# Kernel tuning notes

Measured on AMD Instinct MI355X. Metric: run time of the kernel, lower is better.

The kernel has to match this reference:

```python
import jax, jax.numpy as jnp
import numpy as np
from jax import lax

B, T, D, FF, E, TOPK, CLS = 16, 512, 1024, 2048, 4, 2, 1200
KW = 3  # conv kernel width per ff_kernelsize=[3,3]


def _sinusoidal_pe(T, D):
    pos = np.arange(T, dtype=np.float32)[:, None]
    div = np.exp(np.arange(0, D, 2, dtype=np.float32) * (-np.log(10000.0) / D))
    pe = np.zeros((T, D), dtype=np.float32)
    pe[:, 0::2] = np.sin(pos * div)
    pe[:, 1::2] = np.cos(pos * div)
    return jnp.asarray(pe)


def setup_inputs() -> dict:
    key = jax.random.key(0)
    ks = jax.random.split(key, 12)
    sc = 0.02
    x = jax.random.normal(ks[0], (B, T, D), jnp.float32)
    mask = jax.random.randint(ks[1], (B, T), 0, 2).astype(jnp.int32)
    mask = mask.at[:, 0].set(1)  # ensure >=1 valid token
    return {
        "x": x,
        "mask": mask,
        "fc1_w": jax.random.normal(ks[2], (D, D), jnp.float32) * sc,
        "fc1_b": jnp.zeros((D,), jnp.float32),
        "bn_g": jnp.ones((D,), jnp.float32),
        "bn_b": jnp.zeros((D,), jnp.float32),
        "pe": _sinusoidal_pe(T, D),
        "gate_w": jax.random.normal(ks[3], (D, E), jnp.float32) * sc,
        "ew1": jax.random.normal(ks[4], (E, FF, D, KW), jnp.float32) * sc,  # OIH per expert
        "eb1": jnp.zeros((E, FF), jnp.float32),
        "ew2": jax.random.normal(ks[5], (E, D, FF, KW), jnp.float32) * sc,
        "eb2": jnp.zeros((E, D), jnp.float32),
        "ln_g": jnp.ones((D,), jnp.float32),
        "ln_b": jnp.zeros((D,), jnp.float32),
        "out_w": jax.random.normal(ks[6], (CLS, D), jnp.float32) * sc,
        "out_b": jnp.zeros((CLS,), jnp.float32),
    }


def _forward(x, mask, fc1_w, fc1_b, bn_g, bn_b, pe, gate_w, ew1, eb1, ew2, eb2, ln_g, ln_b, out_w, out_b):
    mf = mask.astype(x.dtype)[..., None]  # [B,T,1]

    # fc1
    h = jnp.einsum("btd,ed->bte", x, fc1_w) + fc1_b

    # MaskedNorm (batch): stats over valid tokens only, invalid positions passed through
    cnt = jnp.maximum(jnp.sum(mf), 1.0)
    mean = jnp.sum(h * mf, axis=(0, 1)) / cnt
    var = jnp.sum(mf * (h - mean) ** 2, axis=(0, 1)) / cnt
    normed = (h - mean) * lax.rsqrt(var + 1e-5) * bn_g + bn_b
    h = jnp.where(mf > 0, normed, h)

    # ReLU + positional encoding (+ dropout is identity in eval)
    h = jax.nn.relu(h) + pe[None, :, :]

    # --- MoE with top-2 gating over 4 conv-FFN experts ---
    logits_g = jnp.einsum("btd,de->bte", h, gate_w)  # [B,T,E]
    probs_g = jax.nn.softmax(logits_g, axis=-1)
    top_v, top_i = lax.top_k(logits_g, TOPK)  # [B,T,K]
    top_g = jax.nn.softmax(top_v, axis=-1)
    # scatter top-k gates into dense [B,T,E] (E=4, cheap)
    gates = jnp.sum(top_g[..., None] * jax.nn.one_hot(top_i, E, dtype=h.dtype), axis=2)

    ht = jnp.transpose(h, (0, 2, 1))  # [B,D,T] for NCH conv

    def expert(w1, b1, w2, b2):
        y = lax.conv_general_dilated(ht, w1, (1,), "SAME", dimension_numbers=("NCH", "OIH", "NCH"))
        y = jax.nn.relu(y + b1[None, :, None])
        y = lax.conv_general_dilated(y, w2, (1,), "SAME", dimension_numbers=("NCH", "OIH", "NCH"))
        return y + b2[None, :, None]  # [B,D,T]

    ys = jax.vmap(expert)(ew1, eb1, ew2, eb2)  # [E,B,D,T]
    moe_out = jnp.einsum("bte,ebdt->btd", gates, ys)

    # load-balancing aux loss (Switch-style)
    frac = jnp.mean((gates > 0).astype(h.dtype), axis=(0, 1))  # tokens per expert
    imp = jnp.mean(probs_g, axis=(0, 1))
    aux_loss = E * jnp.sum(frac * imp)

    # LayerNorm (eps 1e-6)
    mu = jnp.mean(moe_out, axis=-1, keepdims=True)
    v = jnp.mean((moe_out - mu) ** 2, axis=-1, keepdims=True)
    feat = (moe_out - mu) * lax.rsqrt(v + 1e-6) * ln_g + ln_b

    logits = jnp.einsum("btd,cd->btc", feat, out_w) + out_b
    logp = jax.nn.log_softmax(logits, axis=2)
    p = jnp.exp(logp)
    feat_norm = feat / jnp.maximum(jnp.linalg.norm(feat, axis=-1, keepdims=True), 1e-12)
    return feat, feat_norm, logits, logp, p, aux_loss


def reference(x, mask, fc1_w, fc1_b, bn_g, bn_b, pe, gate_w, ew1, eb1, ew2, eb2, ln_g, ln_b, out_w, out_b):
    return _forward(x, mask, fc1_w, fc1_b, bn_g, bn_b, pe, gate_w, ew1, eb1, ew2, eb2, ln_g, ln_b, out_w, out_b)
```

## Files before the change

kernel.cpp:

```cpp
#include <hip/hip_runtime.h>
#include <hip/hip_bf16.h>


namespace {

constexpr int kB = 16, kT = 512, kD = 1024, kFF = 2048, kE = 4, kCLS = 1200;
constexpr int kM = kB * kT;
constexpr int kTP = kT + 2;
constexpr int kCLSP = 1280;
constexpr size_t kBTD = (size_t)kM * kD;
constexpr size_t kBTC = (size_t)kM * kCLS;
constexpr size_t kY1S = (size_t)kB * kTP * kFF;
constexpr size_t kTapStride = (size_t)kFF * kD;

constexpr size_t WS_H     = 0;
constexpr size_t WS_HPAD  = WS_H + kBTD;
constexpr size_t WS_Y1P   = WS_HPAD + (size_t)kB * kTP * kD / 2;
constexpr size_t WS_W1T   = WS_Y1P + (size_t)kB * kTP * kFF / 2;
constexpr size_t WS_W2T   = WS_W1T + (size_t)3 * kFF * kD / 2;
constexpr size_t WS_GATES = WS_W2T + (size_t)3 * kD * kFF / 2;
constexpr size_t WS_PROBS = WS_GATES + (size_t)kM * kE;
constexpr size_t WS_W1HI  = WS_PROBS + (size_t)kM * kE;
constexpr size_t WS_W1LO  = WS_W1HI + (size_t)kD * kD / 2;
constexpr size_t WS_OWB   = WS_W1LO + (size_t)kD * kD / 2;
constexpr size_t WS_SUMS  = WS_OWB + (size_t)kCLSP * kD / 2;
constexpr size_t WS_SUMSQ = WS_SUMS + kD;
constexpr size_t WS_CNT   = WS_SUMSQ + kD;
constexpr size_t WS_AA    = WS_CNT + 1;
constexpr size_t WS_CC    = WS_AA + kD;
constexpr int WS_ZERON = (int)(2 * kD + 1);

constexpr size_t BW_H     = 0;
constexpr size_t BW_HPAD  = BW_H + kBTD;
constexpr size_t BW_Y1    = BW_HPAD + (size_t)kB * kTP * kD / 2;
constexpr size_t BW_W1T   = BW_Y1 + (size_t)kE * kY1S / 2;
constexpr size_t BW_W2T   = BW_W1T + (size_t)kE * 3 * kFF * kD / 2;
constexpr size_t BW_GATES = BW_W2T + (size_t)kE * 3 * kD * kFF / 2;
constexpr size_t BW_PROBS = BW_GATES + (size_t)kM * kE;
constexpr size_t BW_W1HI  = BW_PROBS + (size_t)kM * kE;
constexpr size_t BW_W1LO  = BW_W1HI + (size_t)kD * kD / 2;
constexpr size_t BW_OWB   = BW_W1LO + (size_t)kD * kD / 2;
constexpr size_t BW_SUMS  = BW_OWB + (size_t)kCLSP * kD / 2;
constexpr size_t BW_SUMSQ = BW_SUMS + kD;
constexpr size_t BW_CNT   = BW_SUMSQ + kD;
constexpr size_t BW_AA    = BW_CNT + 1;
constexpr size_t BW_CC    = BW_AA + kD;
constexpr size_t BW_ECNT  = BW_CC + kD;
constexpr size_t BW_ELIST = BW_ECNT + 4;
constexpr size_t BW_END   = BW_ELIST + (size_t)kE * kM;

typedef __attribute__((ext_vector_type(8))) short short8;
typedef __attribute__((ext_vector_type(4))) float f32x4;

#define GLOBAL_LOAD_LDS16(gp, lp)                                          \
  __builtin_amdgcn_global_load_lds(                                        \
      (const __attribute__((address_space(1))) void*)(gp),                 \
      (__attribute__((address_space(3))) void*)(lp), 16, 0, 0)

__device__ __forceinline__ float block_reduce_sum(float v, float* red) {
  const int tid = threadIdx.x;
  __syncthreads();
  red[tid] = v;
  __syncthreads();
  for (int s = 128; s > 0; s >>= 1) {
    if (tid < s) red[tid] += red[tid + s];
    __syncthreads();
  }
  return red[0];
}

__device__ __forceinline__ float block_reduce_max(float v, float* red) {
  const int tid = threadIdx.x;
  __syncthreads();
  red[tid] = v;
  __syncthreads();
  for (int s = 128; s > 0; s >>= 1) {
    if (tid < s) red[tid] = fmaxf(red[tid], red[tid + s]);
    __syncthreads();
  }
  return red[0];
}

__global__ void k_zero(float* __restrict__ p, int n) {
  int i = blockIdx.x * 256 + threadIdx.x;
  if (i < n) p[i] = 0.f;
}

__global__ void k_zero_bnd(__hip_bfloat16* __restrict__ Hpad,
                           __hip_bfloat16* __restrict__ Y1pad) {
  const int b = blockIdx.x >> 1;
  const int row = b * kTP + ((blockIdx.x & 1) ? (kTP - 1) : 0);
  const __hip_bfloat16 z = __float2bfloat16(0.f);
  for (int d = threadIdx.x; d < kD; d += 256) Hpad[(size_t)row * kD + d] = z;
  for (int d = threadIdx.x; d < kFF; d += 256) Y1pad[(size_t)row * kFF + d] = z;
}

__global__ void k_zero_bnd_all(__hip_bfloat16* __restrict__ Hpad,
                               __hip_bfloat16* __restrict__ Y1all) {
  const int g = blockIdx.x;
  const int which = g / (2 * kB);
  const int r = g % (2 * kB);
  const int b = r >> 1;
  const int row = b * kTP + ((r & 1) ? (kTP - 1) : 0);
  const __hip_bfloat16 z = __float2bfloat16(0.f);
  if (which == 0) {
    for (int d = threadIdx.x; d < kD; d += 256) Hpad[(size_t)row * kD + d] = z;
  } else {
    __hip_bfloat16* Y = Y1all + (size_t)(which - 1) * kY1S;
    for (int d = threadIdx.x; d < kFF; d += 256) Y[(size_t)row * kFF + d] = z;
  }
}

__global__ __launch_bounds__(256) void k_split(const float* __restrict__ src,
                                               __hip_bfloat16* __restrict__ hi,
                                               __hip_bfloat16* __restrict__ lo,
                                               int n4) {
  const int i = blockIdx.x * 256 + threadIdx.x;
  if (i >= n4) return;
  const float4 v = *reinterpret_cast<const float4*>(src + (size_t)i * 4);
  const float vv[4] = {v.x, v.y, v.z, v.w};
  unsigned short h[4], l[4];
#pragma unroll
  for (int j = 0; j < 4; ++j) {
    __hip_bfloat16 hb = __float2bfloat16(vv[j]);
    __hip_bfloat16 lb = __float2bfloat16(vv[j] - __bfloat162float(hb));
    h[j] = *reinterpret_cast<unsigned short*>(&hb);
    l[j] = *reinterpret_cast<unsigned short*>(&lb);
  }
  *reinterpret_cast<short4*>(hi + (size_t)i * 4) =
      make_short4(h[0], h[1], h[2], h[3]);
  *reinterpret_cast<short4*>(lo + (size_t)i * 4) =
      make_short4(l[0], l[1], l[2], l[3]);
}

__global__ __launch_bounds__(256) void k_wcast_pad(
    const float* __restrict__ w, __hip_bfloat16* __restrict__ dst) {
  const size_t i = (size_t)blockIdx.x * 256 + threadIdx.x;
  if (i >= (size_t)kCLSP * kD) return;
  const size_t r = i / kD;
  dst[i] = __float2bfloat16(r < kCLS ? w[i] : 0.f);
}

__global__ __launch_bounds__(256) void k_wt(const float* __restrict__ src,
                                            __hip_bfloat16* __restrict__ dst,
                                            int n) {
  const int i = blockIdx.x * 256 + threadIdx.x;
  if (i >= n) return;
  const float* s = src + (size_t)i * 3;
  dst[i] = __float2bfloat16(s[0]);
  dst[(size_t)n + i] = __float2bfloat16(s[1]);
  dst[(size_t)2 * n + i] = __float2bfloat16(s[2]);
}

__global__ __launch_bounds__(256) void k_wt_all(const float* __restrict__ ew1,
                                                const float* __restrict__ ew2,
                                                __hip_bfloat16* __restrict__ W1T,
                                                __hip_bfloat16* __restrict__ W2T) {
  const size_t n = (size_t)kFF * kD;
  const size_t total = (size_t)kE * n;
  const size_t i = (size_t)blockIdx.x * 256 + threadIdx.x;
  if (i >= total) return;
  const size_t e = i / n, j = i - e * n;
  {
    const float* s = ew1 + (e * n + j) * 3;
    __hip_bfloat16* d = W1T + e * 3 * n;
    d[j] = __float2bfloat16(s[0]);
    d[n + j] = __float2bfloat16(s[1]);
    d[2 * n + j] = __float2bfloat16(s[2]);
  }
  {
    const float* s = ew2 + (e * n + j) * 3;
    __hip_bfloat16* d = W2T + e * 3 * n;
    d[j] = __float2bfloat16(s[0]);
    d[n + j] = __float2bfloat16(s[1]);
    d[2 * n + j] = __float2bfloat16(s[2]);
  }
}

__global__ __launch_bounds__(256) void k_build_elist(
    const float* __restrict__ gates, int* __restrict__ elist,
    int* __restrict__ ecnt) {
  __shared__ int red[256];
  const int e = blockIdx.x;
  const int tid = threadIdx.x;
  const int base = tid * 32;
  int cnt = 0;
  for (int j = 0; j < 32; ++j)
    if (gates[(size_t)(base + j) * 4 + e] > 0.f) ++cnt;
  red[tid] = cnt;
  __syncthreads();
  for (int s = 1; s < 256; s <<= 1) {
    const int v = (tid >= s) ? red[tid - s] : 0;
    __syncthreads();
    red[tid] += v;
    __syncthreads();
  }
  const int total = red[255];
  int pos = red[tid] - cnt;
  int* dst = elist + (size_t)e * kM;
  for (int j = 0; j < 32; ++j) {
    const int tk = base + j;
    if (gates[(size_t)tk * 4 + e] > 0.f) dst[pos++] = tk;
  }
  const int padded = (total + 255) & ~255;
  for (int i = total + tid; i < padded; i += 256) dst[i] = 0;
  if (tid == 0) ecnt[e] = total;
}

__global__ __launch_bounds__(256) void k_fc1_mfma(
    const __hip_bfloat16* __restrict__ Xhi, const __hip_bfloat16* __restrict__ Xlo,
    const __hip_bfloat16* __restrict__ Whi, const __hip_bfloat16* __restrict__ Wlo,
    const float* __restrict__ bias, float* __restrict__ H) {
  __shared__ __align__(16) __hip_bfloat16 As[128 * 32];
  __shared__ __align__(16) __hip_bfloat16 Bs[128 * 32];
  const int tid = threadIdx.x;
  const int m0 = blockIdx.y * 128;
  const int n0 = blockIdx.x * 128;
  const int w = tid >> 6, lane = tid & 63;
  const int wm = (w >> 1) * 64, wn = (w & 1) * 64;
  f32x4 acc[4][4] = {};
  const int fr = lane & 15, fc = (lane >> 4) * 8;
  const __hip_bfloat16* Aps[3] = {Xhi, Xlo, Xhi};
  const __hip_bfloat16* Bps[3] = {Whi, Whi, Wlo};
  for (int p = 0; p < 3; ++p) {
    const __hip_bfloat16* Ab = Aps[p] + (size_t)m0 * kD;
    const __hip_bfloat16* Bb = Bps[p] + (size_t)n0 * kD;
    for (int k0 = 0; k0 < kD; k0 += 32) {
      __syncthreads();
#pragma unroll
      for (int r = 0; r < 2; ++r) {
        const int idx = r * 256 + tid;
        const int row = idx >> 2, cg = (idx & 3) * 8;
        GLOBAL_LOAD_LDS16(Ab + (size_t)row * kD + k0 + cg, &As[idx * 8]);
        GLOBAL_LOAD_LDS16(Bb + (size_t)row * kD + k0 + cg, &Bs[idx * 8]);
      }
      __syncthreads();
      short8 af[4], bf[4];
#pragma unroll
      for (int i = 0; i < 4; ++i) {
        af[i] = *reinterpret_cast<const short8*>(&As[(wm + i * 16 + fr) * 32 + fc]);
        bf[i] = *reinterpret_cast<const short8*>(&Bs[(wn + i * 16 + fr) * 32 + fc]);
      }
#pragma unroll
      for (int i = 0; i < 4; ++i)
#pragma unroll
        for (int j = 0; j < 4; ++j)
          acc[i][j] = __builtin_amdgcn_mfma_f32_16x16x32_bf16(af[i], bf[j], acc[i][j], 0, 0, 0);
    }
  }
  const int cr = (lane >> 4) * 4, cc = lane & 15;
#pragma unroll
  for (int i = 0; i < 4; ++i) {
#pragma unroll
    for (int r = 0; r < 4; ++r) {
      const int m = m0 + wm + i * 16 + cr + r;
#pragma unroll
      for (int j = 0; j < 4; ++j) {
        const int gc = n0 + wn + j * 16 + cc;
        H[(size_t)m * kD + gc] = acc[i][j][r] + bias[gc];
      }
    }
  }
}

__global__ __launch_bounds__(256) void k_cls_mfma(
    const __hip_bfloat16* __restrict__ Fb, const __hip_bfloat16* __restrict__ Wb,
    const float* __restrict__ bias, float* __restrict__ logits) {
  __shared__ __align__(16) __hip_bfloat16 As[128 * 32];
  __shared__ __align__(16) __hip_bfloat16 Bs[128 * 32];
  const int tid = threadIdx.x;
  const int m0 = blockIdx.y * 128;
  const int n0 = blockIdx.x * 128;
  const int w = tid >> 6, lane = tid & 63;
  const int wm = (w >> 1) * 64, wn = (w & 1) * 64;
  f32x4 acc[4][4] = {};
  const int fr = lane & 15, fc = (lane >> 4) * 8;
  const __hip_bfloat16* Ab = Fb + (size_t)m0 * kD;
  const __hip_bfloat16* Bb = Wb + (size_t)n0 * kD;
  for (int k0 = 0; k0 < kD; k0 += 32) {
    __syncthreads();
#pragma unroll
    for (int r = 0; r < 2; ++r) {
      const int idx = r * 256 + tid;
      const int row = idx >> 2, cg = (idx & 3) * 8;
      GLOBAL_LOAD_LDS16(Ab + (size_t)row * kD + k0 + cg, &As[idx * 8]);
      GLOBAL_LOAD_LDS16(Bb + (size_t)row * kD + k0 + cg, &Bs[idx * 8]);
    }
    __syncthreads();
    short8 af[4], bf[4];
#pragma unroll
    for (int i = 0; i < 4; ++i) {
      af[i] = *reinterpret_cast<const short8*>(&As[(wm + i * 16 + fr) * 32 + fc]);
      bf[i] = *reinterpret_cast<const short8*>(&Bs[(wn + i * 16 + fr) * 32 + fc]);
    }
#pragma unroll
    for (int i = 0; i < 4; ++i)
#pragma unroll
      for (int j = 0; j < 4; ++j)
        acc[i][j] = __builtin_amdgcn_mfma_f32_16x16x32_bf16(af[i], bf[j], acc[i][j], 0, 0, 0);
  }
  const int cr = (lane >> 4) * 4, cc = lane & 15;
#pragma unroll
  for (int i = 0; i < 4; ++i) {
#pragma unroll
    for (int r = 0; r < 4; ++r) {
      const int m = m0 + wm + i * 16 + cr + r;
#pragma unroll
      for (int j = 0; j < 4; ++j) {
        const int gc = n0 + wn + j * 16 + cc;
        if (gc < kCLS) logits[(size_t)m * kCLS + gc] = acc[i][j][r] + bias[gc];
      }
    }
  }
}

__global__ __launch_bounds__(256) void k_conv1_mfma(
    const __hip_bfloat16* __restrict__ Hpad, const __hip_bfloat16* __restrict__ W1T,
    const float* __restrict__ b1, __hip_bfloat16* __restrict__ Y1pad) {
  __shared__ __align__(16) __hip_bfloat16 As[128 * 32];
  __shared__ __align__(16) __hip_bfloat16 Bs[128 * 32];
  const int tid = threadIdx.x;
  const int m0 = blockIdx.y * 128;
  const int n0 = blockIdx.x * 128;
  const int b = m0 >> 9;
  const int t0 = m0 & (kT - 1);
  const int arow0 = b * kTP + t0;
  const int w = tid >> 6, lane = tid & 63;
  const int wm = (w >> 1) * 64, wn = (w & 1) * 64;
  f32x4 acc[4][4] = {};
  const int fr = lane & 15, fc = (lane >> 4) * 8;
  for (int kk = 0; kk < 3; ++kk) {
    const __hip_bfloat16* Ab = Hpad + (size_t)(arow0 + kk) * kD;
    const __hip_bfloat16* Bb = W1T + (size_t)kk * kFF * kD + (size_t)n0 * kD;
    for (int k0 = 0; k0 < kD; k0 += 32) {
      __syncthreads();
#pragma unroll
      for (int r = 0; r < 2; ++r) {
        const int idx = r * 256 + tid;
        const int row = idx >> 2, cg = (idx & 3) * 8;
        GLOBAL_LOAD_LDS16(Ab + (size_t)row * kD + k0 + cg, &As[idx * 8]);
        GLOBAL_LOAD_LDS16(Bb + (size_t)row * kD + k0 + cg, &Bs[idx * 8]);
      }
      __syncthreads();
      short8 af[4], bf[4];
#pragma unroll
      for (int i = 0; i < 4; ++i) {
        af[i] = *reinterpret_cast<const short8*>(&As[(wm + i * 16 + fr) * 32 + fc]);
        bf[i] = *reinterpret_cast<const short8*>(&Bs[(wn + i * 16 + fr) * 32 + fc]);
      }
#pragma unroll
      for (int i = 0; i < 4; ++i)
#pragma unroll
        for (int j = 0; j < 4; ++j)
          acc[i][j] = __builtin_amdgcn_mfma_f32_16x16x32_bf16(af[i], bf[j], acc[i][j], 0, 0, 0);
    }
  }
  const int orow0 = b * kTP + t0 + 1;
  const int cr = (lane >> 4) * 4, cc = lane & 15;
#pragma unroll
  for (int i = 0; i < 4; ++i) {
#pragma unroll
    for (int r = 0; r < 4; ++r) {
      const int lr = wm + i * 16 + cr + r;
#pragma unroll
      for (int j = 0; j < 4; ++j) {
        const int gc = n0 + wn + j * 16 + cc;
        const float v = acc[i][j][r] + b1[gc];
        Y1pad[(size_t)(orow0 + lr) * kFF + gc] = __float2bfloat16(fmaxf(v, 0.f));
      }
    }
  }
}

__global__ __launch_bounds__(256) void k_conv2_mfma(
    const __hip_bfloat16* __restrict__ Y1pad, const __hip_bfloat16* __restrict__ W2T,
    const float* __restrict__ b2, const float* __restrict__ gates,
    int e, float* __restrict__ moe) {
  __shared__ __align__(16) __hip_bfloat16 As[128 * 32];
  __shared__ __align__(16) __hip_bfloat16 Bs[128 * 32];
  const int tid = threadIdx.x;
  const int m0 = blockIdx.y * 128;
  const int n0 = blockIdx.x * 128;
  const int b = m0 >> 9;
  const int t0 = m0 & (kT - 1);
  const int arow0 = b * kTP + t0;
  const int w = tid >> 6, lane = tid & 63;
  const int wm = (w >> 1) * 64, wn = (w & 1) * 64;
  f32x4 acc[4][4] = {};
  const int fr = lane & 15, fc = (lane >> 4) * 8;
  for (int kk = 0; kk < 3; ++kk) {
    const __hip_bfloat16* Ab = Y1pad + (size_t)(arow0 + kk) * kFF;
    const __hip_bfloat16* Bb = W2T + (size_t)kk * kD * kFF + (size_t)n0 * kFF;
    for (int k0 = 0; k0 < kFF; k0 += 32) {
      __syncthreads();
#pragma unroll
      for (int r = 0; r < 2; ++r) {
        const int idx = r * 256 + tid;
        const int row = idx >> 2, cg = (idx & 3) * 8;
        GLOBAL_LOAD_LDS16(Ab + (size_t)row * kFF + k0 + cg, &As[idx * 8]);
        GLOBAL_LOAD_LDS16(Bb + (size_t)row * kFF + k0 + cg, &Bs[idx * 8]);
      }
      __syncthreads();
      short8 af[4], bf[4];
#pragma unroll
      for (int i = 0; i < 4; ++i) {
        af[i] = *reinterpret_cast<const short8*>(&As[(wm + i * 16 + fr) * 32 + fc]);
        bf[i] = *reinterpret_cast<const short8*>(&Bs[(wn + i * 16 + fr) * 32 + fc]);
      }
#pragma unroll
      for (int i = 0; i < 4; ++i)
#pragma unroll
        for (int j = 0; j < 4; ++j)
          acc[i][j] = __builtin_amdgcn_mfma_f32_16x16x32_bf16(af[i], bf[j], acc[i][j], 0, 0, 0);
    }
  }
  const int cr = (lane >> 4) * 4, cc = lane & 15;
#pragma unroll
  for (int i = 0; i < 4; ++i) {
#pragma unroll
    for (int r = 0; r < 4; ++r) {
      const int lr = wm + i * 16 + cr + r;
      const int m = m0 + lr;
      const float g = gates[(size_t)m * kE + e];
#pragma unroll
      for (int j = 0; j < 4; ++j) {
        const int gc = n0 + wn + j * 16 + cc;
        const float v = acc[i][j][r] + b2[gc];
        const size_t idx = (size_t)m * kD + gc;
        moe[idx] = (e == 0 ? 0.f : moe[idx]) + g * v;
      }
    }
  }
}

#define WAITBAR(N)                                  \
  do {                                              \
    asm volatile("s_waitcnt vmcnt(" #N ")");        \
    __builtin_amdgcn_s_barrier();                   \
    __builtin_amdgcn_sched_barrier(0);              \
  } while (0)

#define QUAD(D, MH, NH, LOADA)                                                \
  do {                                                                        \
    const int _d = (D);                                                       \
    if (LOADA) {                                                              \
      const int _ab = ((_d * 2 + (MH)) << 14) + (fr << 6) + (fc << 1);        \
      _Pragma("unroll") for (int _i = 0; _i < 4; ++_i)                        \
          _Pragma("unroll") for (int _ks = 0; _ks < 2; ++_ks)                 \
              areg[_i][_ks] = *reinterpret_cast<const short8*>(               \
                  smem + ((_ab + (((wr * 4 + _i) * 2 + _ks) << 10)) ^ aswz)); \
    }                                                                         \
    short8 breg[2][2];                                                        \
    const int _bb =                                                           \
        65536 + ((_d * 2 + (NH)) << 14) + (fr << 6) + (fc << 1);              \
    _Pragma("unroll") for (int _j = 0; _j < 2; ++_j)                          \
        _Pragma("unroll") for (int _ks = 0; _ks < 2; ++_ks)                   \
            breg[_j][_ks] = *reinterpret_cast<const short8*>(                 \
                smem + ((_bb + (((wc * 2 + _j) * 2 + _ks) << 10)) ^ aswz));   \
    __builtin_amdgcn_s_setprio(1);                                            \
    _Pragma("unroll") for (int _i = 0; _i < 4; ++_i)                          \
        _Pragma("unroll") for (int _j = 0; _j < 2; ++_j)                      \
            _Pragma("unroll") for (int _ks = 0; _ks < 2; ++_ks)               \
                acc[MH][NH][_i][_j] =                                         \
                    __builtin_amdgcn_mfma_f32_16x16x32_bf16(                  \
                        areg[_i][_ks], breg[_j][_ks], acc[MH][NH][_i][_j],    \
                        0, 0, 0);                                             \
    __builtin_amdgcn_s_setprio(0);                                            \
  } while (0)

template <int K1, bool CONV1>
__global__ __launch_bounds__(512, 2) void k_conv8ph(
    const __hip_bfloat16* __restrict__ Asrc,
    const __hip_bfloat16* __restrict__ Wt,
    const float* __restrict__ bias,
    const float* __restrict__ gates,
    __hip_bfloat16* __restrict__ Yout,
    float* __restrict__ moe) {
  constexpr int NTOT = CONV1 ? kFF : kD;
  constexpr int NX = NTOT / 256;
  constexpr int NY = kM / 256;
  constexpr int NWG = kE * NY * NX;
  constexpr int KT1 = K1 / 64;
  constexpr int NT = 3 * KT1;
  extern __shared__ __align__(16) char smem[];

  int lid = blockIdx.x;
  lid = (lid & 7) * (NWG / 8) + (lid >> 3);
  const int e = lid / (NY * NX);
  const int rem = lid - e * (NY * NX);
  const int by = rem / NX, bx = rem - by * NX;
  const int m0 = by * 256, n0 = bx * 256;
  const int b = m0 >> 9, t0 = m0 & (kT - 1);
  const int arow0 = b * kTP + t0;

  const int tid = threadIdx.x;
  const int w = tid >> 6, l = tid & 63;
  const int wr = w >> 2, wc = w & 3;
  const int fr = l & 15, fc = (l >> 4) << 3;
  const int aswz = (fr & 8) ? 32 : 0;
  const int srr = l >> 2;
  const int scc = ((l & 3) << 3) ^ ((l & 32) ? 16 : 0);

  const __hip_bfloat16* Apan =
      (CONV1 ? Asrc : (Asrc + (size_t)e * kY1S)) + (size_t)arow0 * K1;
  const __hip_bfloat16* Bpan = Wt + (size_t)e * 3 * kTapStride + (size_t)n0 * K1;

  auto stageA = [&](int tau, int d, int mh) {
    const int kk = tau / KT1, kf = (tau % KT1) << 6;
    const __hip_bfloat16* org = Apan + (size_t)(kk + mh * 128) * K1 + kf;
    const int lb = (d * 2 + mh) << 14;
#pragma unroll
    for (int r = 0; r < 2; ++r) {
      const int s = w + r * 8;
      GLOBAL_LOAD_LDS16(org + (size_t)((s >> 1) * 16 + srr) * K1 +
                            ((s & 1) << 5) + scc,
                        smem + lb + (s << 10));
    }
  };
  auto stageB = [&](int tau, int d, int nh) {
    const int kk = tau / KT1, kf = (tau % KT1) << 6;
    const __hip_bfloat16* org =
        Bpan + (size_t)kk * kTapStride + (size_t)(nh * 128) * K1 + kf;
    const int lb = 65536 + ((d * 2 + nh) << 14);
#pragma unroll
    for (int r = 0; r < 2; ++r) {
      const int s = w + r * 8;
      GLOBAL_LOAD_LDS16(org + (size_t)((s >> 1) * 16 + srr) * K1 +
                            ((s & 1) << 5) + scc,
                        smem + lb + (s << 10));
    }
  };

  f32x4 acc[2][2][4][2] = {};
  short8 areg[4][2];

  stageA(0, 0, 0);
  stageB(0, 0, 0);
  stageB(0, 0, 1);
  stageA(0, 0, 1);

  for (int tau = 0; tau < NT - 1; ++tau) {
    const int d = tau & 1, dn = d ^ 1;
    WAITBAR(4); stageA(tau + 1, dn, 0); QUAD(d, 0, 0, true);
    WAITBAR(4); stageB(tau + 1, dn, 0); QUAD(d, 0, 1, false);
    WAITBAR(4); stageB(tau + 1, dn, 1); QUAD(d, 1, 0, true);
                stageA(tau + 1, dn, 1); QUAD(d, 1, 1, false);
  }
  {
    const int d = (NT - 1) & 1;
    WAITBAR(4); QUAD(d, 0, 0, true);
    WAITBAR(2); QUAD(d, 0, 1, false);
    WAITBAR(0); QUAD(d, 1, 0, true);
                QUAD(d, 1, 1, false);
  }

  const int cr = (l >> 4) * 4, cc = l & 15;
  if (CONV1) {
    __hip_bfloat16* Yb = Yout + (size_t)e * kY1S;
    const float* be = bias + (size_t)e * kFF;
    const int orow0 = b * kTP + t0 + 1;
#pragma unroll
    for (int mh = 0; mh < 2; ++mh)
#pragma unroll
      for (int i = 0; i < 4; ++i)
#pragma unroll
        for (int r = 0; r < 4; ++r) {
          const int rl = mh * 128 + wr * 64 + i * 16 + cr + r;
#pragma unroll
          for (int nh = 0; nh < 2; ++nh)
#pragma unroll
            for (int j = 0; j < 2; ++j) {
              const int gc = n0 + nh * 128 + wc * 32 + j * 16 + cc;
              const float v = acc[mh][nh][i][j][r] + be[gc];
              Yb[(size_t)(orow0 + rl) * kFF + gc] =
                  __float2bfloat16(fmaxf(v, 0.f));
            }
        }
  } else {
    const float* be = bias + (size_t)e * kD;
#pragma unroll
    for (int mh = 0; mh < 2; ++mh)
#pragma unroll
      for (int i = 0; i < 4; ++i)
#pragma unroll
        for (int r = 0; r < 4; ++r) {
          const int rl = mh * 128 + wr * 64 + i * 16 + cr + r;
          const int m = m0 + rl;
          const float g = gates[(size_t)m * kE + e];
#pragma unroll
          for (int nh = 0; nh < 2; ++nh)
#pragma unroll
            for (int j = 0; j < 2; ++j) {
              const int gc = n0 + nh * 128 + wc * 32 + j * 16 + cc;
              const float v = acc[mh][nh][i][j][r] + be[gc];
              atomicAdd(&moe[(size_t)m * kD + gc], g * v);
            }
        }
  }
}

__global__ __launch_bounds__(512, 2) void k_conv2sp(
    const __hip_bfloat16* __restrict__ Y1all,
    const __hip_bfloat16* __restrict__ W2T,
    const float* __restrict__ b2, const float* __restrict__ gates,
    const int* __restrict__ elist, const int* __restrict__ ecnt,
    float* __restrict__ moe) {
  constexpr int K1 = kFF;
  constexpr int NX = kD / 256;
  constexpr int NY = kM / 256;
  constexpr int NWG = kE * NY * NX;
  constexpr int KT1 = K1 / 64;
  constexpr int NT = 3 * KT1;
  extern __shared__ __align__(16) char smem[];

  int lid = blockIdx.x;
  lid = (lid & 7) * (NWG / 8) + (lid >> 3);
  const int e = lid / (NY * NX);
  const int rem = lid - e * (NY * NX);
  const int by = rem / NX, bx = rem - by * NX;
  const int m0 = by * 256, n0 = bx * 256;
  const int cnt_e = ecnt[e];
  if (m0 >= cnt_e) return;

  const int tid = threadIdx.x;
  const int w = tid >> 6, l = tid & 63;
  const int wr = w >> 2, wc = w & 3;
  const int fr = l & 15, fc = (l >> 4) << 3;
  const int aswz = (fr & 8) ? 32 : 0;
  const int srr = l >> 2;
  const int scc = ((l & 3) << 3) ^ ((l & 32) ? 16 : 0);

  const int* el = elist + (size_t)e * kM + m0;
  const __hip_bfloat16* Ye = Y1all + (size_t)e * kY1S;
  const __hip_bfloat16* Bpan =
      W2T + (size_t)e * 3 * kTapStride + (size_t)n0 * K1;

  const int colbits = ((w & 1) << 5) + scc;
  const int r0 = (w >> 1) * 16 + srr;
  const int r1 = r0 + 64;
  const __hip_bfloat16* aptr[2][2];
#pragma unroll
  for (int mh = 0; mh < 2; ++mh) {
    const int tk0 = el[mh * 128 + r0];
    const int tk1 = el[mh * 128 + r1];
    aptr[mh][0] = Ye +
        (size_t)((tk0 >> 9) * kTP + (tk0 & (kT - 1))) * K1 + colbits;
    aptr[mh][1] = Ye +
        (size_t)((tk1 >> 9) * kTP + (tk1 & (kT - 1))) * K1 + colbits;
  }

  auto stageA = [&](int tau, int d, int mh) {
    const int lb = (d * 2 + mh) << 14;
    GLOBAL_LOAD_LDS16(aptr[mh][0] + tau * 64, smem + lb + (w << 10));
    GLOBAL_LOAD_LDS16(aptr[mh][1] + tau * 64, smem + lb + ((w + 8) << 10));
  };
  auto stageB = [&](int tau, int d, int nh) {
    const int kk = tau / KT1, kf = (tau % KT1) << 6;
    const __hip_bfloat16* org =
        Bpan + (size_t)kk * kTapStride + (size_t)(nh * 128) * K1 + kf;
    const int lb = 65536 + ((d * 2 + nh) << 14);
#pragma unroll
    for (int r = 0; r < 2; ++r) {
      const int s = w + r * 8;
      GLOBAL_LOAD_LDS16(org + (size_t)((s >> 1) * 16 + srr) * K1 +
                            ((s & 1) << 5) + scc,
                        smem + lb + (s << 10));
    }
  };

  f32x4 acc[2][2][4][2] = {};
  short8 areg[4][2];

  stageA(0, 0, 0);
  stageB(0, 0, 0);
  stageB(0, 0, 1);
  stageA(0, 0, 1);

  for (int tau = 0; tau < NT - 1; ++tau) {
    const int d = tau & 1, dn = d ^ 1;
    WAITBAR(4); stageA(tau + 1, dn, 0); QUAD(d, 0, 0, true);
    WAITBAR(4); stageB(tau + 1, dn, 0); QUAD(d, 0, 1, false);
    WAITBAR(4); stageB(tau + 1, dn, 1); QUAD(d, 1, 0, true);
                stageA(tau + 1, dn, 1); QUAD(d, 1, 1, false);
  }
  {
    const int d = (NT - 1) & 1;
    WAITBAR(4); QUAD(d, 0, 0, true);
    WAITBAR(2); QUAD(d, 0, 1, false);
    WAITBAR(0); QUAD(d, 1, 0, true);
                QUAD(d, 1, 1, false);
  }

  const int cr = (l >> 4) * 4, cc = l & 15;
  const float* be = b2 + (size_t)e * kD;
#pragma unroll
  for (int mh = 0; mh < 2; ++mh)
#pragma unroll
    for (int i = 0; i < 4; ++i)
#pragma unroll
      for (int r = 0; r < 4; ++r) {
        const int rl = mh * 128 + wr * 64 + i * 16 + cr + r;
        if (m0 + rl < cnt_e) {
          const int tk = el[rl];
          const float g = gates[(size_t)tk * 4 + e];
#pragma unroll
          for (int nh = 0; nh < 2; ++nh)
#pragma unroll
            for (int j = 0; j < 2; ++j) {
              const int gc = n0 + nh * 128 + wc * 32 + j * 16 + cc;
              const float v = acc[mh][nh][i][j][r] + be[gc];
              atomicAdd(&moe[(size_t)tk * kD + gc], g * v);
            }
        }
      }
}

__global__ __launch_bounds__(256) void k_cnt(const int* __restrict__ mask,
                                             float* __restrict__ cnt) {
  __shared__ float red[256];
  const int i = blockIdx.x * 256 + threadIdx.x;
  float v = (float)mask[i];
  v = block_reduce_sum(v, red);
  if (threadIdx.x == 0) atomicAdd(cnt, v);
}

__global__ __launch_bounds__(256) void k_stats(const float* __restrict__ H,
                                               const int* __restrict__ mask,
                                               float* __restrict__ sums,
                                               float* __restrict__ sumsq) {
  const int ch = blockIdx.x * 256 + threadIdx.x;
  const int r0 = blockIdx.y * 64;
  float s = 0.f, q = 0.f;
  for (int r = r0; r < r0 + 64; ++r) {
    if (mask[r]) {
      const float v = H[(size_t)r * kD + ch];
      s += v;
      q += v * v;
    }
  }
  atomicAdd(&sums[ch], s);
  atomicAdd(&sumsq[ch], q);
}

__global__ __launch_bounds__(256) void k_finalize(
    const float* __restrict__ sums, const float* __restrict__ sumsq,
    const float* __restrict__ cntp, const float* __restrict__ bn_g,
    const float* __restrict__ bn_b, float* __restrict__ aa,
    float* __restrict__ cc) {
  const int d = blockIdx.x * 256 + threadIdx.x;
  const float cnt = fmaxf(*cntp, 1.f);
  const float mean = sums[d] / cnt;
  const float var = sumsq[d] / cnt - mean * mean;
  const float istd = rsqrtf(var + 1e-5f);
  const float a = bn_g[d] * istd;
  aa[d] = a;
  cc[d] = bn_b[d] - mean * a;
}

__global__ __launch_bounds__(256) void k_norm_gate(
    const float* __restrict__ H, const int* __restrict__ mask,
    const float* __restrict__ pe, const float* __restrict__ aa,
    const float* __restrict__ cc, const float* __restrict__ gw,
    __hip_bfloat16* __restrict__ Hpad, float* __restrict__ gates,
    float* __restrict__ probs) {
  __shared__ float red[256];
  __shared__ float glog[4];
  const int r = blockIdx.x;
  const int tid = threadIdx.x;
  const int b = r >> 9;
  const int t = r & (kT - 1);
  const bool mv = mask[r] != 0;
  const size_t orow = (size_t)(b * kTP + t + 1) * kD;
  float gl[4] = {0.f, 0.f, 0.f, 0.f};
#pragma unroll
  for (int j = 0; j < 4; ++j) {
    const int d = tid + j * 256;
    float v = H[(size_t)r * kD + d];
    if (mv) v = v * aa[d] + cc[d];
    v = fmaxf(v, 0.f) + pe[(size_t)t * kD + d];
    Hpad[orow + d] = __float2bfloat16(v);
    const float4 g = *reinterpret_cast<const float4*>(gw + (size_t)d * 4);
    gl[0] += v * g.x; gl[1] += v * g.y; gl[2] += v * g.z; gl[3] += v * g.w;
  }
  for (int e = 0; e < 4; ++e) {
    const float s = block_reduce_sum(gl[e], red);
    if (tid == 0) glog[e] = s;
  }
  __syncthreads();
  if (tid == 0) {
    float lg[4] = {glog[0], glog[1], glog[2], glog[3]};
    const float mx = fmaxf(fmaxf(lg[0], lg[1]), fmaxf(lg[2], lg[3]));
    float ex[4], s = 0.f;
#pragma unroll
    for (int e = 0; e < 4; ++e) { ex[e] = expf(lg[e] - mx); s += ex[e]; }
    int i0 = 0;
    for (int e = 1; e < 4; ++e) if (lg[e] > lg[i0]) i0 = e;
    int i1 = -1;
    for (int e = 0; e < 4; ++e) {
      if (e == i0) continue;
      if (i1 < 0 || lg[e] > lg[i1]) i1 = e;
    }
    const float g0 = 1.f / (1.f + expf(lg[i1] - lg[i0]));
    float gv[4] = {0.f, 0.f, 0.f, 0.f};
    gv[i0] = g0;
    gv[i1] = 1.f - g0;
    *reinterpret_cast<float4*>(gates + (size_t)r * 4) =
        make_float4(gv[0], gv[1], gv[2], gv[3]);
    const float inv_s = 1.f / s;
    *reinterpret_cast<float4*>(probs + (size_t)r * 4) =
        make_float4(ex[0] * inv_s, ex[1] * inv_s, ex[2] * inv_s, ex[3] * inv_s);
  }
}

__global__ __launch_bounds__(256) void k_ln(
    const float* __restrict__ moe, const float* __restrict__ g,
    const float* __restrict__ b, float* __restrict__ feat,
    float* __restrict__ featn, __hip_bfloat16* __restrict__ featb) {
  __shared__ float red[256];
  const int r = blockIdx.x;
  const int tid = threadIdx.x;
  float v[4];
  float s = 0.f, q = 0.f;
#pragma unroll
  for (int j = 0; j < 4; ++j) {
    v[j] = moe[(size_t)r * kD + tid + j * 256];
    s += v[j];
    q += v[j] * v[j];
  }
  const float sum = block_reduce_sum(s, red);
  const float mu = sum * (1.f / kD);
  const float sq = block_reduce_sum(q, red);
  const float var = sq * (1.f / kD) - mu * mu;
  const float istd = rsqrtf(var + 1e-6f);
  float f[4];
  float fs = 0.f;
#pragma unroll
  for (int j = 0; j < 4; ++j) {
    const int d = tid + j * 256;
    f[j] = (v[j] - mu) * istd * g[d] + b[d];
    feat[(size_t)r * kD + d] = f[j];
    featb[(size_t)r * kD + d] = __float2bfloat16(f[j]);
    fs += f[j] * f[j];
  }
  const float nrm2 = block_reduce_sum(fs, red);
  const float scale = 1.f / fmaxf(sqrtf(nrm2), 1e-12f);
#pragma unroll
  for (int j = 0; j < 4; ++j) {
    const int d = tid + j * 256;
    featn[(size_t)r * kD + d] = f[j] * scale;
  }
}

__global__ __launch_bounds__(256) void k_softmax(
    const float* __restrict__ logits, float* __restrict__ logp,
    float* __restrict__ p) {
  __shared__ float red[256];
  const int r = blockIdx.x;
  const int tid = threadIdx.x;
  float lv[5];
  float mx = -1e30f;
#pragma unroll
  for (int j = 0; j < 5; ++j) {
    const int c = tid + j * 256;
    if (c < kCLS) {
      lv[j] = logits[(size_t)r * kCLS + c];
      mx = fmaxf(mx, lv[j]);
    }
  }
  mx = block_reduce_max(mx, red);
  float s = 0.f;
#pragma unroll
  for (int j = 0; j < 5; ++j) {
    const int c = tid + j * 256;
    if (c < kCLS) s += expf(lv[j] - mx);
  }
  s = block_reduce_sum(s, red);
  const float lse = mx + logf(s);
#pragma unroll
  for (int j = 0; j < 5; ++j) {
    const int c = tid + j * 256;
    if (c < kCLS) {
      const float lp = lv[j] - lse;
      logp[(size_t)r * kCLS + c] = lp;
      p[(size_t)r * kCLS + c] = expf(lp);
    }
  }
}

__global__ __launch_bounds__(256) void k_aux(const float* __restrict__ probs,
                                             const float* __restrict__ gates,
                                             float* __restrict__ out) {
  __shared__ float red[256];
  const int tid = threadIdx.x;
  float si[4] = {0.f, 0.f, 0.f, 0.f};
  float sf[4] = {0.f, 0.f, 0.f, 0.f};
  for (int i = tid; i < kM; i += 256) {
    const float4 p = *reinterpret_cast<const float4*>(probs + (size_t)i * 4);
    const float4 g = *reinterpret_cast<const float4*>(gates + (size_t)i * 4);
    si[0] += p.x; si[1] += p.y; si[2] += p.z; si[3] += p.w;
    sf[0] += (g.x > 0.f) ? 1.f : 0.f;
    sf[1] += (g.y > 0.f) ? 1.f : 0.f;
    sf[2] += (g.z > 0.f) ? 1.f : 0.f;
    sf[3] += (g.w > 0.f) ? 1.f : 0.f;
  }
  float tot = 0.f;
  for (int e = 0; e < 4; ++e) {
    const float S = block_reduce_sum(si[e], red);
    const float F = block_reduce_sum(sf[e], red);
    tot += (F / (float)kM) * (S / (float)kM);
  }
  if (tid == 0) out[0] = (float)kE * tot;
}

}

extern "C" void kernel_launch(void* const* d_in, const int* in_sizes, int n_in,
                              void* d_out, int out_size, void* d_ws,
                              size_t ws_size, hipStream_t stream) {
  const float* x     = (const float*)d_in[0];
  const int*   mask  = (const int*)d_in[1];
  const float* fc1_w = (const float*)d_in[2];
  const float* fc1_b = (const float*)d_in[3];
  const float* bn_g  = (const float*)d_in[4];
  const float* bn_b  = (const float*)d_in[5];
  const float* pe    = (const float*)d_in[6];
  const float* gw    = (const float*)d_in[7];
  const float* ew1   = (const float*)d_in[8];
  const float* eb1   = (const float*)d_in[9];
  const float* ew2   = (const float*)d_in[10];
  const float* eb2   = (const float*)d_in[11];
  const float* ln_g  = (const float*)d_in[12];
  const float* ln_b  = (const float*)d_in[13];
  const float* out_w = (const float*)d_in[14];
  const float* out_b = (const float*)d_in[15];

  float* ws = (float*)d_ws;

  float* outf   = (float*)d_out;
  float* feat   = outf;
  float* featn  = outf + kBTD;
  float* logits = outf + 2 * kBTD;
  float* logp   = logits + kBTC;
  float* pprob  = logp + kBTC;
  float* aux    = pprob + kBTC;

  const bool batched = ws_size >= BW_END * sizeof(float);

  if (batched) {
    float* H     = ws + BW_H;
    __hip_bfloat16* HPAD  = (__hip_bfloat16*)(ws + BW_HPAD);
    __hip_bfloat16* Y1ALL = (__hip_bfloat16*)(ws + BW_Y1);
    __hip_bfloat16* XHI   = Y1ALL;
    __hip_bfloat16* XLO   = XHI + kBTD;
    __hip_bfloat16* FEATB = Y1ALL;
    __hip_bfloat16* W1T   = (__hip_bfloat16*)(ws + BW_W1T);
    __hip_bfloat16* W2T   = (__hip_bfloat16*)(ws + BW_W2T);
    float* GATES = ws + BW_GATES;
    float* PROBS = ws + BW_PROBS;
    __hip_bfloat16* W1HI = (__hip_bfloat16*)(ws + BW_W1HI);
    __hip_bfloat16* W1LO = (__hip_bfloat16*)(ws + BW_W1LO);
    __hip_bfloat16* OWB  = (__hip_bfloat16*)(ws + BW_OWB);
    float* SUMS  = ws + BW_SUMS;
    int*   ECNT  = (int*)(ws + BW_ECNT);
    int*   ELIST = (int*)(ws + BW_ELIST);
    float* MOE   = H;

    k_zero<<<dim3((WS_ZERON + 255) / 256), 256, 0, stream>>>(SUMS, WS_ZERON);
    k_split<<<dim3((int)(kBTD / 4 + 255) / 256), 256, 0, stream>>>(
        x, XHI, XLO, (int)(kBTD / 4));
    k_split<<<dim3((kD * kD / 4 + 255) / 256), 256, 0, stream>>>(
        fc1_w, W1HI, W1LO, kD * kD / 4);
    k_fc1_mfma<<<dim3(kD / 128, kM / 128), 256, 0, stream>>>(
        XHI, XLO, W1HI, W1LO, fc1_b, H);
    k_zero_bnd_all<<<dim3(2 * kB * (1 + kE)), 256, 0, stream>>>(HPAD, Y1ALL);
    k_wt_all<<<dim3((int)(((size_t)kE * kFF * kD + 255) / 256)), 256, 0,
               stream>>>(ew1, ew2, W1T, W2T);
    k_cnt<<<dim3(kM / 256), 256, 0, stream>>>(mask, ws + BW_CNT);
    k_stats<<<dim3(kD / 256, kM / 64), 256, 0, stream>>>(H, mask, SUMS,
                                                         ws + BW_SUMSQ);
    k_finalize<<<dim3(kD / 256), 256, 0, stream>>>(
        SUMS, ws + BW_SUMSQ, ws + BW_CNT, bn_g, bn_b, ws + BW_AA, ws + BW_CC);
    k_norm_gate<<<dim3(kM), 256, 0, stream>>>(H, mask, pe, ws + BW_AA,
                                              ws + BW_CC, gw, HPAD, GATES,
                                              PROBS);
    k_build_elist<<<dim3(kE), 256, 0, stream>>>(GATES, ELIST, ECNT);
    k_zero<<<dim3((int)((kBTD + 255) / 256)), 256, 0, stream>>>(MOE,
                                                                (int)kBTD);
    k_conv8ph<kD, true><<<dim3(kE * (kM / 256) * (kFF / 256)), 512, 131072,
                          stream>>>(HPAD, W1T, eb1, nullptr, Y1ALL, nullptr);
    k_conv2sp<<<dim3(kE * (kM / 256) * (kD / 256)), 512, 131072, stream>>>(
        Y1ALL, W2T, eb2, GATES, ELIST, ECNT, MOE);
    k_ln<<<dim3(kM), 256, 0, stream>>>(MOE, ln_g, ln_b, feat, featn, FEATB);
    k_wcast_pad<<<dim3((int)((size_t)kCLSP * kD + 255) / 256), 256, 0,
                  stream>>>(out_w, OWB);
    k_cls_mfma<<<dim3(kCLSP / 128, kM / 128), 256, 0, stream>>>(FEATB, OWB,
                                                                out_b, logits);
    k_softmax<<<dim3(kM), 256, 0, stream>>>(logits, logp, pprob);
    k_aux<<<1, 256, 0, stream>>>(PROBS, GATES, aux);
    return;
  }

  float* H     = ws + WS_H;
  __hip_bfloat16* HPAD  = (__hip_bfloat16*)(ws + WS_HPAD);
  __hip_bfloat16* Y1PAD = (__hip_bfloat16*)(ws + WS_Y1P);
  __hip_bfloat16* XHI   = (__hip_bfloat16*)(ws + WS_Y1P);
  __hip_bfloat16* XLO   = XHI + kBTD;
  __hip_bfloat16* FEATB = (__hip_bfloat16*)(ws + WS_Y1P);
  __hip_bfloat16* W1T   = (__hip_bfloat16*)(ws + WS_W1T);
  __hip_bfloat16* W2T   = (__hip_bfloat16*)(ws + WS_W2T);
  float* GATES = ws + WS_GATES;
  float* PROBS = ws + WS_PROBS;
  __hip_bfloat16* W1HI = (__hip_bfloat16*)(ws + WS_W1HI);
  __hip_bfloat16* W1LO = (__hip_bfloat16*)(ws + WS_W1LO);
  __hip_bfloat16* OWB  = (__hip_bfloat16*)(ws + WS_OWB);
  float* SUMS  = ws + WS_SUMS;
  float* SUMSQ = ws + WS_SUMSQ;
  float* CNT   = ws + WS_CNT;
  float* AA    = ws + WS_AA;
  float* CC    = ws + WS_CC;
  float* MOE   = H;

  k_zero<<<dim3((WS_ZERON + 255) / 256), 256, 0, stream>>>(SUMS, WS_ZERON);
  k_split<<<dim3((int)(kBTD / 4 + 255) / 256), 256, 0, stream>>>(x, XHI, XLO,
                                                                 (int)(kBTD / 4));
  k_split<<<dim3((kD * kD / 4 + 255) / 256), 256, 0, stream>>>(
      fc1_w, W1HI, W1LO, kD * kD / 4);
  k_fc1_mfma<<<dim3(kD / 128, kM / 128), 256, 0, stream>>>(XHI, XLO, W1HI,
                                                           W1LO, fc1_b, H);
  k_zero_bnd<<<dim3(2 * kB), 256, 0, stream>>>(HPAD, Y1PAD);
  k_cnt<<<dim3(kM / 256), 256, 0, stream>>>(mask, CNT);
  k_stats<<<dim3(kD / 256, kM / 64), 256, 0, stream>>>(H, mask, SUMS, SUMSQ);
  k_finalize<<<dim3(kD / 256), 256, 0, stream>>>(SUMS, SUMSQ, CNT, bn_g, bn_b,
                                                 AA, CC);
  k_norm_gate<<<dim3(kM), 256, 0, stream>>>(H, mask, pe, AA, CC, gw, HPAD,
                                            GATES, PROBS);
  for (int e = 0; e < kE; ++e) {
    k_wt<<<dim3((kFF * kD + 255) / 256), 256, 0, stream>>>(
        ew1 + (size_t)e * kFF * kD * 3, W1T, kFF * kD);
    k_wt<<<dim3((kD * kFF + 255) / 256), 256, 0, stream>>>(
        ew2 + (size_t)e * kD * kFF * 3, W2T, kD * kFF);
    k_conv1_mfma<<<dim3(kFF / 128, kM / 128), 256, 0, stream>>>(
        HPAD, W1T, eb1 + (size_t)e * kFF, Y1PAD);
    k_conv2_mfma<<<dim3(kD / 128, kM / 128), 256, 0, stream>>>(
        Y1PAD, W2T, eb2 + (size_t)e * kD, GATES, e, MOE);
  }
  k_ln<<<dim3(kM), 256, 0, stream>>>(MOE, ln_g, ln_b, feat, featn, FEATB);
  k_wcast_pad<<<dim3((int)((size_t)kCLSP * kD + 255) / 256), 256, 0, stream>>>(
      out_w, OWB);
  k_cls_mfma<<<dim3(kCLSP / 128, kM / 128), 256, 0, stream>>>(FEATB, OWB,
                                                              out_b, logits);
  k_softmax<<<dim3(kM), 256, 0, stream>>>(logits, logp, pprob);
  k_aux<<<1, 256, 0, stream>>>(PROBS, GATES, aux);
}
```

Measured before the change: 1.409 ms.

## Split conv2 into per-tap tasks scheduled by persistent work-queue blocks

Replaces the fixed grid for the second expert conv, which launched tiles for every expert and exited early for empty ones, with a compacted task list built on device and consumed by 256 persistent blocks through an atomic counter. Each tile is also split into three per-tap tasks with shorter K loops, adding the bias only on the center tap. This aims to remove idle early-exit blocks and balance load across CUs. In exchange the atomicAdd traffic into the output triples, and each task pays its own pipeline prologue and epilogue.

```diff
diff --git a/kernel.cpp b/kernel.cpp
--- a/kernel.cpp
+++ b/kernel.cpp
@@ -47,7 +47,9 @@
 constexpr size_t BW_CC    = BW_AA + kD;
 constexpr size_t BW_ECNT  = BW_CC + kD;
 constexpr size_t BW_ELIST = BW_ECNT + 4;
-constexpr size_t BW_END   = BW_ELIST + (size_t)kE * kM;
+constexpr size_t BW_META  = BW_ELIST + (size_t)kE * kM;
+constexpr size_t BW_TASKS = BW_META + 4;
+constexpr size_t BW_END   = BW_TASKS + 1024;
 
 typedef __attribute__((ext_vector_type(8))) short short8;
 typedef __attribute__((ext_vector_type(4))) float f32x4;
@@ -205,6 +207,33 @@
   const int padded = (total + 255) & ~255;
   for (int i = total + tid; i < padded; i += 256) dst[i] = 0;
   if (tid == 0) ecnt[e] = total;
+}
+
+__global__ __launch_bounds__(256) void k_build_tasks(
+    const int* __restrict__ ecnt, int* __restrict__ tasks,
+    int* __restrict__ meta) {
+  __shared__ int off[5];
+  const int tid = threadIdx.x;
+  if (tid == 0) {
+    off[0] = 0;
+    for (int e = 0; e < 4; ++e)
+      off[e + 1] = off[e] + (ecnt[e] + 255) / 256;
+    meta[0] = off[4] * 4 * 3;
+    meta[1] = 0;
+  }
+  __syncthreads();
+  const int nmt = off[4];
+  const int np = nmt * 4;
+  for (int i = tid; i < nmt; i += 256) {
+    int e = 0;
+    while (off[e + 1] <= i) ++e;
+    const int mt = i - off[e];
+    for (int nx = 0; nx < 4; ++nx) {
+      const int code_base = e * 128 + mt * 4 + nx;
+      for (int tap = 0; tap < 3; ++tap)
+        tasks[tap * np + i * 4 + nx] = code_base + (tap << 9);
+    }
+  }
 }
 
 __global__ __launch_bounds__(256) void k_fc1_mfma(
@@ -599,28 +628,17 @@
   }
 }
 
-__global__ __launch_bounds__(512, 2) void k_conv2sp(
+__global__ __launch_bounds__(512, 2) void k_conv2q(
     const __hip_bfloat16* __restrict__ Y1all,
     const __hip_bfloat16* __restrict__ W2T,
     const float* __restrict__ b2, const float* __restrict__ gates,
     const int* __restrict__ elist, const int* __restrict__ ecnt,
+    const int* __restrict__ tasks, int* __restrict__ meta,
     float* __restrict__ moe) {
   constexpr int K1 = kFF;
-  constexpr int NX = kD / 256;
-  constexpr int NY = kM / 256;
-  constexpr int NWG = kE * NY * NX;
-  constexpr int KT1 = K1 / 64;
-  constexpr int NT = 3 * KT1;
+  constexpr int NT = K1 / 64;
   extern __shared__ __align__(16) char smem[];
-
-  int lid = blockIdx.x;
-  lid = (lid & 7) * (NWG / 8) + (lid >> 3);
-  const int e = lid / (NY * NX);
-  const int rem = lid - e * (NY * NX);
-  const int by = rem / NX, bx = rem - by * NX;
-  const int m0 = by * 256, n0 = bx * 256;
-  const int cnt_e = ecnt[e];
-  if (m0 >= cnt_e) return;
+  int* sbc = (int*)(smem + 131072);
 
   const int tid = threadIdx.x;
   const int w = tid >> 6, l = tid & 63;
@@ -629,90 +647,106 @@
   const int aswz = (fr & 8) ? 32 : 0;
   const int srr = l >> 2;
   const int scc = ((l & 3) << 3) ^ ((l & 32) ? 16 : 0);
-
-  const int* el = elist + (size_t)e * kM + m0;
-  const __hip_bfloat16* Ye = Y1all + (size_t)e * kY1S;
-  const __hip_bfloat16* Bpan =
-      W2T + (size_t)e * 3 * kTapStride + (size_t)n0 * K1;
-
   const int colbits = ((w & 1) << 5) + scc;
   const int r0 = (w >> 1) * 16 + srr;
   const int r1 = r0 + 64;
-  const __hip_bfloat16* aptr[2][2];
-#pragma unroll
-  for (int mh = 0; mh < 2; ++mh) {
-    const int tk0 = el[mh * 128 + r0];
-    const int tk1 = el[mh * 128 + r1];
-    aptr[mh][0] = Ye +
-        (size_t)((tk0 >> 9) * kTP + (tk0 & (kT - 1))) * K1 + colbits;
-    aptr[mh][1] = Ye +
-        (size_t)((tk1 >> 9) * kTP + (tk1 & (kT - 1))) * K1 + colbits;
-  }
-
-  auto stageA = [&](int tau, int d, int mh) {
-    const int lb = (d * 2 + mh) << 14;
-    GLOBAL_LOAD_LDS16(aptr[mh][0] + tau * 64, smem + lb + (w << 10));
-    GLOBAL_LOAD_LDS16(aptr[mh][1] + tau * 64, smem + lb + ((w + 8) << 10));
-  };
-  auto stageB = [&](int tau, int d, int nh) {
-    const int kk = tau / KT1, kf = (tau % KT1) << 6;
-    const __hip_bfloat16* org =
-        Bpan + (size_t)kk * kTapStride + (size_t)(nh * 128) * K1 + kf;
-    const int lb = 65536 + ((d * 2 + nh) << 14);
-#pragma unroll
-    for (int r = 0; r < 2; ++r) {
-      const int s = w + r * 8;
-      GLOBAL_LOAD_LDS16(org + (size_t)((s >> 1) * 16 + srr) * K1 +
-                            ((s & 1) << 5) + scc,
-                        smem + lb + (s << 10));
-    }
-  };
-
-  f32x4 acc[2][2][4][2] = {};
-  short8 areg[4][2];
-
-  stageA(0, 0, 0);
-  stageB(0, 0, 0);
-  stageB(0, 0, 1);
-  stageA(0, 0, 1);
-
-  for (int tau = 0; tau < NT - 1; ++tau) {
-    const int d = tau & 1, dn = d ^ 1;
-    WAITBAR(4); stageA(tau + 1, dn, 0); QUAD(d, 0, 0, true);
-    WAITBAR(4); stageB(tau + 1, dn, 0); QUAD(d, 0, 1, false);
-    WAITBAR(4); stageB(tau + 1, dn, 1); QUAD(d, 1, 0, true);
-                stageA(tau + 1, dn, 1); QUAD(d, 1, 1, false);
-  }
-  {
-    const int d = (NT - 1) & 1;
-    WAITBAR(4); QUAD(d, 0, 0, true);
-    WAITBAR(2); QUAD(d, 0, 1, false);
-    WAITBAR(0); QUAD(d, 1, 0, true);
-                QUAD(d, 1, 1, false);
-  }
-
-  const int cr = (l >> 4) * 4, cc = l & 15;
-  const float* be = b2 + (size_t)e * kD;
-#pragma unroll
-  for (int mh = 0; mh < 2; ++mh)
-#pragma unroll
-    for (int i = 0; i < 4; ++i)
-#pragma unroll
-      for (int r = 0; r < 4; ++r) {
-        const int rl = mh * 128 + wr * 64 + i * 16 + cr + r;
-        if (m0 + rl < cnt_e) {
-          const int tk = el[rl];
-          const float g = gates[(size_t)tk * 4 + e];
-#pragma unroll
-          for (int nh = 0; nh < 2; ++nh)
-#pragma unroll
-            for (int j = 0; j < 2; ++j) {
-              const int gc = n0 + nh * 128 + wc * 32 + j * 16 + cc;
-              const float v = acc[mh][nh][i][j][r] + be[gc];
-              atomicAdd(&moe[(size_t)tk * kD + gc], g * v);
-            }
+  const int ntasks = meta[0];
+
+  for (;;) {
+    if (tid == 0) sbc[0] = atomicAdd(&meta[1], 1);
+    __syncthreads();
+    const int task = sbc[0];
+    if (task >= ntasks) return;
+    const int code = tasks[task];
+    const int nx = code & 3;
+    const int mt = (code >> 2) & 31;
+    const int e = (code >> 7) & 3;
+    const int tap = code >> 9;
+    const int m0 = mt * 256, n0 = nx * 256;
+    const int cnt_e = ecnt[e];
+
+    const int* el = elist + (size_t)e * kM + m0;
+    const __hip_bfloat16* Ye = Y1all + (size_t)e * kY1S;
+    const __hip_bfloat16* Bpan =
+        W2T + ((size_t)e * 3 + tap) * kTapStride + (size_t)n0 * K1;
+
+    const __hip_bfloat16* aptr[2][2];
+#pragma unroll
+    for (int mh = 0; mh < 2; ++mh) {
+      const int tk0 = el[mh * 128 + r0];
+      const int tk1 = el[mh * 128 + r1];
+      aptr[mh][0] = Ye +
+          (size_t)((tk0 >> 9) * kTP + (tk0 & (kT - 1)) + tap) * K1 + colbits;
+      aptr[mh][1] = Ye +
+          (size_t)((tk1 >> 9) * kTP + (tk1 & (kT - 1)) + tap) * K1 + colbits;
+    }
+
+    auto stageA = [&](int tau, int d, int mh) {
+      const int lb = (d * 2 + mh) << 14;
+      GLOBAL_LOAD_LDS16(aptr[mh][0] + tau * 64, smem + lb + (w << 10));
+      GLOBAL_LOAD_LDS16(aptr[mh][1] + tau * 64, smem + lb + ((w + 8) << 10));
+    };
+    auto stageB = [&](int tau, int d, int nh) {
+      const __hip_bfloat16* org =
+          Bpan + (size_t)(nh * 128) * K1 + (tau << 6);
+      const int lb = 65536 + ((d * 2 + nh) << 14);
+#pragma unroll
+      for (int r = 0; r < 2; ++r) {
+        const int s = w + r * 8;
+        GLOBAL_LOAD_LDS16(org + (size_t)((s >> 1) * 16 + srr) * K1 +
+                              ((s & 1) << 5) + scc,
+                          smem + lb + (s << 10));
+      }
+    };
+
+    f32x4 acc[2][2][4][2] = {};
+    short8 areg[4][2];
+
+    stageA(0, 0, 0);
+    stageB(0, 0, 0);
+    stageB(0, 0, 1);
+    stageA(0, 0, 1);
+
+    for (int tau = 0; tau < NT - 1; ++tau) {
+      const int d = tau & 1, dn = d ^ 1;
+      WAITBAR(4); stageA(tau + 1, dn, 0); QUAD(d, 0, 0, true);
+      WAITBAR(4); stageB(tau + 1, dn, 0); QUAD(d, 0, 1, false);
+      WAITBAR(4); stageB(tau + 1, dn, 1); QUAD(d, 1, 0, true);
+                  stageA(tau + 1, dn, 1); QUAD(d, 1, 1, false);
+    }
+    {
+      const int d = (NT - 1) & 1;
+      WAITBAR(4); QUAD(d, 0, 0, true);
+      WAITBAR(2); QUAD(d, 0, 1, false);
+      WAITBAR(0); QUAD(d, 1, 0, true);
+                  QUAD(d, 1, 1, false);
+    }
+
+    const int cr = (l >> 4) * 4, cc = l & 15;
+    const float* be = b2 + (size_t)e * kD;
+    const bool addb = (tap == 1);
+#pragma unroll
+    for (int mh = 0; mh < 2; ++mh)
+#pragma unroll
+      for (int i = 0; i < 4; ++i)
+#pragma unroll
+        for (int r = 0; r < 4; ++r) {
+          const int rl = mh * 128 + wr * 64 + i * 16 + cr + r;
+          if (m0 + rl < cnt_e) {
+            const int tk = el[rl];
+            const float g = gates[(size_t)tk * 4 + e];
+#pragma unroll
+            for (int nh = 0; nh < 2; ++nh)
+#pragma unroll
+              for (int j = 0; j < 2; ++j) {
+                const int gc = n0 + nh * 128 + wc * 32 + j * 16 + cc;
+                const float v =
+                    acc[mh][nh][i][j][r] + (addb ? be[gc] : 0.f);
+                atomicAdd(&moe[(size_t)tk * kD + gc], g * v);
+              }
+          }
         }
-      }
+  }
 }
 
 __global__ __launch_bounds__(256) void k_cnt(const int* __restrict__ mask,
@@ -963,6 +997,8 @@
     float* SUMS  = ws + BW_SUMS;
     int*   ECNT  = (int*)(ws + BW_ECNT);
     int*   ELIST = (int*)(ws + BW_ELIST);
+    int*   META  = (int*)(ws + BW_META);
+    int*   TASKS = (int*)(ws + BW_TASKS);
     float* MOE   = H;
 
     k_zero<<<dim3((WS_ZERON + 255) / 256), 256, 0, stream>>>(SUMS, WS_ZERON);
@@ -984,12 +1020,14 @@
                                               ws + BW_CC, gw, HPAD, GATES,
                                               PROBS);
     k_build_elist<<<dim3(kE), 256, 0, stream>>>(GATES, ELIST, ECNT);
+    k_build_tasks<<<dim3(1), 256, 0, stream>>>(ECNT, TASKS, META);
     k_zero<<<dim3((int)((kBTD + 255) / 256)), 256, 0, stream>>>(MOE,
                                                                 (int)kBTD);
     k_conv8ph<kD, true><<<dim3(kE * (kM / 256) * (kFF / 256)), 512, 131072,
                           stream>>>(HPAD, W1T, eb1, nullptr, Y1ALL, nullptr);
-    k_conv2sp<<<dim3(kE * (kM / 256) * (kD / 256)), 512, 131072, stream>>>(
-        Y1ALL, W2T, eb2, GATES, ELIST, ECNT, MOE);
+    k_conv2q<<<dim3(256), 512, 131088, stream>>>(Y1ALL, W2T, eb2, GATES,
+                                                 ELIST, ECNT, TASKS, META,
+                                                 MOE);
     k_ln<<<dim3(kM), 256, 0, stream>>>(MOE, ln_g, ln_b, feat, featn, FEATB);
     k_wcast_pad<<<dim3((int)((size_t)kCLSP * kD + 255) / 256), 256, 0,
                   stream>>>(out_w, OWB);
```

Measured after the change: 1.383 ms. About the same (-1.8%).
